# Performance work log

Hardware: AMD Instinct MI355X
Metric: run time of the kernel (lower is better)

The kernel has to match this reference:

```python
import jax, jax.numpy as jnp
import numpy as np

D_IN = 1024
D_OUT = 1024
NUM_HEADS = 16
HEAD_DIM = D_OUT // NUM_HEADS
SCALE = HEAD_DIM ** -0.5


def setup_inputs() -> dict:
    key = jax.random.key(0)
    k_x, k_qkv, k_pw, k_pb = jax.random.split(key, 4)
    B, S = 2, 2048
    x = jax.random.normal(k_x, (B, S, D_IN), dtype=jnp.float32)
    # nn.Linear weights: stored as (out_features, in_features); qkv_bias=False
    w_qkv = jax.random.normal(k_qkv, (3 * D_OUT, D_IN), dtype=jnp.float32) * (D_IN ** -0.5)
    w_proj = jax.random.normal(k_pw, (D_OUT, D_OUT), dtype=jnp.float32) * (D_OUT ** -0.5)
    b_proj = jax.random.normal(k_pb, (D_OUT,), dtype=jnp.float32) * 0.01
    return {"x": x, "w_qkv": w_qkv, "w_proj": w_proj, "b_proj": b_proj}


def reference(x, w_qkv, w_proj, b_proj):
    B, S, _ = x.shape
    # combined QKV projection: (B,S,3*d_out)
    qkv = jnp.einsum('bsd,ed->bse', x, w_qkv)
    qkv = qkv.reshape(B, S, 3, NUM_HEADS, HEAD_DIM)
    qkv = jnp.transpose(qkv, (2, 0, 3, 1, 4))  # (3,B,H,S,hd)
    q, k, v = qkv[0], qkv[1], qkv[2]
    scores = jnp.einsum('bhqd,bhkd->bhqk', q, k)  # (B,H,S,S)
    causal = jnp.triu(jnp.ones((S, S), dtype=bool), k=1)
    # module masks to -inf first, then scales (softmax-equivalent)
    scores = jnp.where(causal, -jnp.inf, scores) * SCALE
    attn = jax.nn.softmax(scores, axis=-1)
    ctx = jnp.einsum('bhqk,bhkd->bhqd', attn, v)
    ctx = jnp.transpose(ctx, (0, 2, 1, 3)).reshape(B, S, D_OUT)
    return jnp.einsum('bsd,ed->bse', ctx, w_proj) + b_proj
```

## Files before the change

### kernel.cpp

```cpp
#include <hip/hip_runtime.h>

#define SEQ    2048
#define NHEAD  16
#define HDIM   64
#define DMODEL 1024
#define BATCH  2

typedef __bf16 bf16;
typedef __bf16 bf16x8 __attribute__((ext_vector_type(8)));
typedef __bf16 bf16x4v __attribute__((ext_vector_type(4)));
typedef float  f32x4  __attribute__((ext_vector_type(4)));

typedef const __attribute__((address_space(1))) void* gas_ptr;
typedef __attribute__((address_space(3))) void*       las_ptr;

__device__ __forceinline__ f32x4 mfma16(bf16x8 a, bf16x8 b, f32x4 c) {
  return __builtin_amdgcn_mfma_f32_16x16x32_bf16(a, b, c, 0, 0, 0);
}

__device__ __forceinline__ void gload_lds16(const void* g, void* l) {
  __builtin_amdgcn_global_load_lds((gas_ptr)(unsigned long long)g,
                                   (las_ptr)(unsigned long long)l, 16, 0, 0);
}

__global__ void convert_all(const float* __restrict__ x, const float* __restrict__ wq,
                            const float* __restrict__ wp, bf16* __restrict__ out) {
  const long long NX = 4194304, NQ = 3145728, NP = 1048576;
  long long i = ((long long)blockIdx.x * blockDim.x + threadIdx.x) * 4;
  if (i >= NX + NQ + NP) return;
  const float* src; long long off;
  if (i < NX)           { src = x;  off = i; }
  else if (i < NX + NQ) { src = wq; off = i - NX; }
  else                  { src = wp; off = i - NX - NQ; }
  float4 f = *reinterpret_cast<const float4*>(src + off);
  bf16x4v r;
  r[0] = (bf16)f.x; r[1] = (bf16)f.y; r[2] = (bf16)f.z; r[3] = (bf16)f.w;
  *reinterpret_cast<bf16x4v*>(out + i) = r;
}

template <int EPI>
__global__ __launch_bounds__(256) void gemm_bt(
    const bf16* __restrict__ A, const bf16* __restrict__ B, int K,
    bf16* __restrict__ q, bf16* __restrict__ k, bf16* __restrict__ v,
    const float* __restrict__ bias, float* __restrict__ out) {
  __shared__ alignas(16) bf16 As[2][128 * 32];
  __shared__ alignas(16) bf16 Bs[2][128 * 32];

  const int tid = threadIdx.x;
  const int l = tid & 63, w = tid >> 6;
  const int lr = l & 15, lg = l >> 4;
  const int wr = (w >> 1) * 64, wc = (w & 1) * 64;
  const long long m0 = (long long)blockIdx.x * 128;
  const long long n0 = (long long)blockIdx.y * 128;
  const int crow = tid >> 2, ccol = (tid & 3) * 8;

  auto stage = [&](int kt, int buf) {
    const bf16* a_src = A + (m0 + crow) * K + (long long)kt * 32 + ccol;
    const bf16* b_src = B + (n0 + crow) * K + (long long)kt * 32 + ccol;
    gload_lds16(a_src,           &As[buf][tid * 8]);
    gload_lds16(a_src + 64LL * K, &As[buf][(tid + 256) * 8]);
    gload_lds16(b_src,           &Bs[buf][tid * 8]);
    gload_lds16(b_src + 64LL * K, &Bs[buf][(tid + 256) * 8]);
  };

  f32x4 acc[4][4];
  const f32x4 fz = {0.f, 0.f, 0.f, 0.f};
#pragma unroll
  for (int m = 0; m < 4; ++m)
#pragma unroll
    for (int n = 0; n < 4; ++n) acc[m][n] = fz;

  stage(0, 0);
  const int nk = K >> 5;
  int cur = 0;
  for (int kt = 0; kt < nk; ++kt) {
    __syncthreads();
    if (kt + 1 < nk) stage(kt + 1, cur ^ 1);
    bf16x8 af[4], bfv[4];
#pragma unroll
    for (int m = 0; m < 4; ++m)
      af[m] = *reinterpret_cast<const bf16x8*>(&As[cur][(wr + m * 16 + lr) * 32 + lg * 8]);
#pragma unroll
    for (int n = 0; n < 4; ++n)
      bfv[n] = *reinterpret_cast<const bf16x8*>(&Bs[cur][(wc + n * 16 + lr) * 32 + lg * 8]);
#pragma unroll
    for (int m = 0; m < 4; ++m)
#pragma unroll
      for (int n = 0; n < 4; ++n) acc[m][n] = mfma16(af[m], bfv[n], acc[m][n]);
    cur ^= 1;
  }

#pragma unroll
  for (int m = 0; m < 4; ++m) {
#pragma unroll
    for (int n = 0; n < 4; ++n) {
#pragma unroll
      for (int j = 0; j < 4; ++j) {
        long long grow = m0 + wr + m * 16 + lg * 4 + j;
        long long gcol = n0 + wc + n * 16 + lr;
        float val = acc[m][n][j];
        if (EPI == 0) {
          int three = (int)(gcol >> 10);
          int rem = (int)(gcol & 1023);
          int h = rem >> 6, d = rem & 63;
          int b = (int)(grow >> 11), s = (int)(grow & 2047);
          int bh = b * NHEAD + h;
          if (three < 2) {
            int dst = ((bh * 128 + (s >> 4)) * 2 + (d >> 5)) * 512 +
                      (s & 15) * 32 + ((d >> 3) & 3) * 8 + (d & 7);
            if (three == 0) q[dst] = (bf16)(val * 0.125f);
            else            k[dst] = (bf16)val;
          } else {
            int dst = (((bh * 4 + (d >> 4)) * 32 + (s >> 6)) * 2 + ((s >> 5) & 1)) * 512 +
                      (d & 15) * 32 + ((s >> 3) & 3) * 8 + (s & 7);
            v[dst] = (bf16)val;
          }
        } else {
          out[grow * 1024 + gcol] = val + bias[gcol];
        }
      }
    }
  }
}

__global__ __launch_bounds__(256, 2) void attn_kernel(
    const bf16* __restrict__ qbuf, const bf16* __restrict__ kbuf,
    const bf16* __restrict__ vbuf, bf16* __restrict__ ctx) {
  const int lid = blockIdx.y * gridDim.x + blockIdx.x;
  const int xcd = lid & 7;
  const int idx = lid >> 3;
  const int bh  = xcd + (idx >> 4) * 8;
  const int p   = idx & 15;
  const int tid = threadIdx.x;
  const int l = tid & 63, w = tid >> 6;
  const int lr = l & 15, lg = l >> 4;
  const int foff = lr * 32 + lg * 8;

  __shared__ alignas(16) bf16 Pl[4][16][72];

  const bf16* Kb = kbuf + bh * 131072 + foff;
  const bf16* Vb = vbuf + bh * 131072 + foff;
  const int b = bh >> 4, h = bh & 15;
  const f32x4 fz = {0.f, 0.f, 0.f, 0.f};

#pragma unroll
  for (int phase = 0; phase < 2; ++phase) {
    const int qg = phase ? (31 - p) : p;
    const int qt16 = qg * 4 + w;
    const int qr0 = qt16 * 16;

    const bf16* Qb = qbuf + (bh * 128 + qt16) * 1024 + foff;
    bf16x8 qf[2];
    qf[0] = *reinterpret_cast<const bf16x8*>(Qb);
    qf[1] = *reinterpret_cast<const bf16x8*>(Qb + 512);

    f32x4 o[4];
    float mrow[4], lrow[4];
#pragma unroll
    for (int nd = 0; nd < 4; ++nd) o[nd] = fz;
#pragma unroll
    for (int j = 0; j < 4; ++j) { mrow[j] = -1e30f; lrow[j] = 0.f; }

    for (int kt = 0; kt <= qg; ++kt) {
      const bool diag = (kt == qg);

      bf16x8 vf[4][2];
#pragma unroll
      for (int nd = 0; nd < 4; ++nd)
#pragma unroll
        for (int kk = 0; kk < 2; ++kk)
          vf[nd][kk] = *reinterpret_cast<const bf16x8*>(
              &Vb[((nd * 32 + kt) * 2 + kk) * 512]);

      bf16x8 kf[4][2];
#pragma unroll
      for (int n = 0; n < 4; ++n)
#pragma unroll
        for (int kk = 0; kk < 2; ++kk)
          kf[n][kk] = *reinterpret_cast<const bf16x8*>(
              &Kb[((kt * 4 + n) * 2 + kk) * 512]);

      f32x4 s4[4];
#pragma unroll
      for (int n = 0; n < 4; ++n)
        s4[n] = mfma16(qf[1], kf[n][1], mfma16(qf[0], kf[n][0], fz));
      if (diag) {
#pragma unroll
        for (int n = 0; n < 4; ++n)
#pragma unroll
          for (int j = 0; j < 4; ++j)
            if (n * 16 + lr > w * 16 + lg * 4 + j) s4[n][j] = -1e30f;
      }

      float pm[4];
#pragma unroll
      for (int j = 0; j < 4; ++j)
        pm[j] = fmaxf(fmaxf(s4[0][j], s4[1][j]), fmaxf(s4[2][j], s4[3][j]));
#pragma unroll
      for (int msk = 1; msk <= 8; msk <<= 1)
#pragma unroll
        for (int j = 0; j < 4; ++j) pm[j] = fmaxf(pm[j], __shfl_xor(pm[j], msk, 64));
      float alpha[4], rs[4];
#pragma unroll
      for (int j = 0; j < 4; ++j) {
        float mn = fmaxf(mrow[j], pm[j]);
        alpha[j] = __expf(mrow[j] - mn);
        mrow[j] = mn;
        rs[j] = 0.f;
      }
#pragma unroll
      for (int n = 0; n < 4; ++n)
#pragma unroll
        for (int j = 0; j < 4; ++j) {
          float pv = __expf(s4[n][j] - mrow[j]);
          s4[n][j] = pv;
          rs[j] += pv;
        }
#pragma unroll
      for (int msk = 1; msk <= 8; msk <<= 1)
#pragma unroll
        for (int j = 0; j < 4; ++j) rs[j] += __shfl_xor(rs[j], msk, 64);
#pragma unroll
      for (int j = 0; j < 4; ++j) lrow[j] = lrow[j] * alpha[j] + rs[j];
#pragma unroll
      for (int nd = 0; nd < 4; ++nd)
#pragma unroll
        for (int j = 0; j < 4; ++j) o[nd][j] *= alpha[j];

#pragma unroll
      for (int n = 0; n < 4; ++n)
#pragma unroll
        for (int j = 0; j < 4; ++j)
          Pl[w][lg * 4 + j][n * 16 + lr] = (bf16)s4[n][j];

#pragma unroll
      for (int kk = 0; kk < 2; ++kk) {
        bf16x8 pf = *reinterpret_cast<const bf16x8*>(&Pl[w][lr][kk * 32 + lg * 8]);
#pragma unroll
        for (int nd = 0; nd < 4; ++nd)
          o[nd] = mfma16(pf, vf[nd][kk], o[nd]);
      }
    }

    float inv[4];
#pragma unroll
    for (int j = 0; j < 4; ++j) inv[j] = 1.0f / lrow[j];
#pragma unroll
    for (int nd = 0; nd < 4; ++nd)
#pragma unroll
      for (int j = 0; j < 4; ++j) {
        int srow = qr0 + lg * 4 + j;
        int d = nd * 16 + lr;
        ctx[((long long)(b * SEQ + srow)) * DMODEL + h * HDIM + d] =
            (bf16)(o[nd][j] * inv[j]);
      }
  }
}

extern "C" void kernel_launch(void* const* d_in, const int* in_sizes, int n_in,
                              void* d_out, int out_size, void* d_ws, size_t ws_size,
                              hipStream_t stream) {
  const float* x      = (const float*)d_in[0];
  const float* w_qkv  = (const float*)d_in[1];
  const float* w_proj = (const float*)d_in[2];
  const float* b_proj = (const float*)d_in[3];
  float* out = (float*)d_out;

  bf16* ws = (bf16*)d_ws;
  bf16* xb     = ws;
  bf16* wqkvb  = xb + 4194304;
  bf16* wprojb = wqkvb + 3145728;
  bf16* qb     = wprojb + 1048576;
  bf16* kb     = qb + 4194304;
  bf16* vb     = kb + 4194304;
  bf16* ctxb   = vb + 4194304;

  convert_all<<<8192, 256, 0, stream>>>(x, w_qkv, w_proj, xb);
  gemm_bt<0><<<dim3(32, 24), 256, 0, stream>>>(xb, wqkvb, 1024, qb, kb, vb, nullptr, nullptr);
  attn_kernel<<<dim3(16, 32), 256, 0, stream>>>(qb, kb, vb, ctxb);
  gemm_bt<1><<<dim3(32, 8), 256, 0, stream>>>(ctxb, wprojb, 1024, nullptr, nullptr, nullptr,
                                              b_proj, out);
}
```

Before: 200.1 us.

## Software-pipeline K/V register loads across a flattened two-phase attention loop

Flattens the two causal query-tile phases into one 33-iteration loop and double-buffers the K and V fragments in registers, loading the next tile's data while the current tile's MFMAs and softmax run. It also defers the cross-lane row-sum reduction to the end of each query tile instead of doing it every iteration. The aim is to hide global load latency and remove per-iteration shuffles, at the cost of twice the register footprint for K/V fragments, which may lower occupancy or cause spills.

```diff
diff --git a/kernel.cpp b/kernel.cpp
--- a/kernel.cpp
+++ b/kernel.cpp
@@ -143,117 +143,135 @@
   const int b = bh >> 4, h = bh & 15;
   const f32x4 fz = {0.f, 0.f, 0.f, 0.f};
 
-#pragma unroll
-  for (int phase = 0; phase < 2; ++phase) {
-    const int qg = phase ? (31 - p) : p;
-    const int qt16 = qg * 4 + w;
-    const int qr0 = qt16 * 16;
-
-    const bf16* Qb = qbuf + (bh * 128 + qt16) * 1024 + foff;
-    bf16x8 qf[2];
-    qf[0] = *reinterpret_cast<const bf16x8*>(Qb);
-    qf[1] = *reinterpret_cast<const bf16x8*>(Qb + 512);
-
-    f32x4 o[4];
-    float mrow[4], lrow[4];
-#pragma unroll
-    for (int nd = 0; nd < 4; ++nd) o[nd] = fz;
-#pragma unroll
-    for (int j = 0; j < 4; ++j) { mrow[j] = -1e30f; lrow[j] = 0.f; }
-
-    for (int kt = 0; kt <= qg; ++kt) {
-      const bool diag = (kt == qg);
-
-      bf16x8 vf[4][2];
+  f32x4 o[4];
+  float mrow[4], lsum[4];
+  bf16x8 qf[2];
+
+  bf16x8 kA[4][2], vA[4][2], kB[4][2], vB[4][2];
+
+#pragma unroll
+  for (int nd = 0; nd < 4; ++nd)
+#pragma unroll
+    for (int kk = 0; kk < 2; ++kk) {
+      vA[nd][kk] = *reinterpret_cast<const bf16x8*>(&Vb[((nd * 32 + 0) * 2 + kk) * 512]);
+      kA[nd][kk] = *reinterpret_cast<const bf16x8*>(&Kb[((0 * 4 + nd) * 2 + kk) * 512]);
+    }
+
+  auto step = [&](bf16x8 (&kc)[4][2], bf16x8 (&vc)[4][2],
+                  bf16x8 (&kn)[4][2], bf16x8 (&vn)[4][2], int i) {
+    const bool in_a = (i <= p);
+    const int qt = in_a ? p : 31 - p;
+    const int kt = in_a ? i : i - p - 1;
+    const bool diag = (kt == qt);
+
+    if (kt == 0) {
+      const int qt16 = qt * 4 + w;
+      const bf16* Qb = qbuf + (bh * 128 + qt16) * 1024 + foff;
+      qf[0] = *reinterpret_cast<const bf16x8*>(Qb);
+      qf[1] = *reinterpret_cast<const bf16x8*>(Qb + 512);
+#pragma unroll
+      for (int nd = 0; nd < 4; ++nd) o[nd] = fz;
+#pragma unroll
+      for (int j = 0; j < 4; ++j) { mrow[j] = -1e30f; lsum[j] = 0.f; }
+    }
+
+    {
+      const int i2 = i + 1;
+      int kt2 = (i2 <= p) ? i2 : i2 - p - 1;
+      if (i2 > 32) kt2 = 0;
 #pragma unroll
       for (int nd = 0; nd < 4; ++nd)
 #pragma unroll
-        for (int kk = 0; kk < 2; ++kk)
-          vf[nd][kk] = *reinterpret_cast<const bf16x8*>(
-              &Vb[((nd * 32 + kt) * 2 + kk) * 512]);
-
-      bf16x8 kf[4][2];
+        for (int kk = 0; kk < 2; ++kk) {
+          vn[nd][kk] = *reinterpret_cast<const bf16x8*>(&Vb[((nd * 32 + kt2) * 2 + kk) * 512]);
+          kn[nd][kk] = *reinterpret_cast<const bf16x8*>(&Kb[((kt2 * 4 + nd) * 2 + kk) * 512]);
+        }
+    }
+
+    f32x4 s4[4];
+#pragma unroll
+    for (int n = 0; n < 4; ++n)
+      s4[n] = mfma16(qf[1], kc[n][1], mfma16(qf[0], kc[n][0], fz));
+    if (diag) {
 #pragma unroll
       for (int n = 0; n < 4; ++n)
 #pragma unroll
-        for (int kk = 0; kk < 2; ++kk)
-          kf[n][kk] = *reinterpret_cast<const bf16x8*>(
-              &Kb[((kt * 4 + n) * 2 + kk) * 512]);
-
-      f32x4 s4[4];
-#pragma unroll
-      for (int n = 0; n < 4; ++n)
-        s4[n] = mfma16(qf[1], kf[n][1], mfma16(qf[0], kf[n][0], fz));
-      if (diag) {
-#pragma unroll
-        for (int n = 0; n < 4; ++n)
-#pragma unroll
-          for (int j = 0; j < 4; ++j)
-            if (n * 16 + lr > w * 16 + lg * 4 + j) s4[n][j] = -1e30f;
+        for (int j = 0; j < 4; ++j)
+          if (n * 16 + lr > w * 16 + lg * 4 + j) s4[n][j] = -1e30f;
+    }
+
+    float pm[4];
+#pragma unroll
+    for (int j = 0; j < 4; ++j)
+      pm[j] = fmaxf(fmaxf(s4[0][j], s4[1][j]), fmaxf(s4[2][j], s4[3][j]));
+#pragma unroll
+    for (int msk = 1; msk <= 8; msk <<= 1)
+#pragma unroll
+      for (int j = 0; j < 4; ++j) pm[j] = fmaxf(pm[j], __shfl_xor(pm[j], msk, 64));
+    float alpha[4];
+#pragma unroll
+    for (int j = 0; j < 4; ++j) {
+      float mn = fmaxf(mrow[j], pm[j]);
+      alpha[j] = __expf(mrow[j] - mn);
+      mrow[j] = mn;
+    }
+    float rs[4] = {0.f, 0.f, 0.f, 0.f};
+#pragma unroll
+    for (int n = 0; n < 4; ++n)
+#pragma unroll
+      for (int j = 0; j < 4; ++j) {
+        float pv = __expf(s4[n][j] - mrow[j]);
+        s4[n][j] = pv;
+        rs[j] += pv;
       }
-
-      float pm[4];
+#pragma unroll
+    for (int j = 0; j < 4; ++j) lsum[j] = lsum[j] * alpha[j] + rs[j];
+#pragma unroll
+    for (int nd = 0; nd < 4; ++nd)
+#pragma unroll
+      for (int j = 0; j < 4; ++j) o[nd][j] *= alpha[j];
+
+#pragma unroll
+    for (int n = 0; n < 4; ++n)
 #pragma unroll
       for (int j = 0; j < 4; ++j)
-        pm[j] = fmaxf(fmaxf(s4[0][j], s4[1][j]), fmaxf(s4[2][j], s4[3][j]));
+        Pl[w][lg * 4 + j][n * 16 + lr] = (bf16)s4[n][j];
+
+#pragma unroll
+    for (int kk = 0; kk < 2; ++kk) {
+      bf16x8 pf = *reinterpret_cast<const bf16x8*>(&Pl[w][lr][kk * 32 + lg * 8]);
+#pragma unroll
+      for (int nd = 0; nd < 4; ++nd)
+        o[nd] = mfma16(pf, vc[nd][kk], o[nd]);
+    }
+
+    if (diag) {
+      float ls[4];
+#pragma unroll
+      for (int j = 0; j < 4; ++j) ls[j] = lsum[j];
 #pragma unroll
       for (int msk = 1; msk <= 8; msk <<= 1)
 #pragma unroll
-        for (int j = 0; j < 4; ++j) pm[j] = fmaxf(pm[j], __shfl_xor(pm[j], msk, 64));
-      float alpha[4], rs[4];
-#pragma unroll
-      for (int j = 0; j < 4; ++j) {
-        float mn = fmaxf(mrow[j], pm[j]);
-        alpha[j] = __expf(mrow[j] - mn);
-        mrow[j] = mn;
-        rs[j] = 0.f;
-      }
-#pragma unroll
-      for (int n = 0; n < 4; ++n)
+        for (int j = 0; j < 4; ++j) ls[j] += __shfl_xor(ls[j], msk, 64);
+      float inv[4];
+#pragma unroll
+      for (int j = 0; j < 4; ++j) inv[j] = 1.0f / ls[j];
+      const int qr0 = (qt * 4 + w) * 16;
+#pragma unroll
+      for (int nd = 0; nd < 4; ++nd)
 #pragma unroll
         for (int j = 0; j < 4; ++j) {
-          float pv = __expf(s4[n][j] - mrow[j]);
-          s4[n][j] = pv;
-          rs[j] += pv;
+          int srow = qr0 + lg * 4 + j;
+          int d = nd * 16 + lr;
+          ctx[((long long)(b * SEQ + srow)) * DMODEL + h * HDIM + d] =
+              (bf16)(o[nd][j] * inv[j]);
         }
-#pragma unroll
-      for (int msk = 1; msk <= 8; msk <<= 1)
-#pragma unroll
-        for (int j = 0; j < 4; ++j) rs[j] += __shfl_xor(rs[j], msk, 64);
-#pragma unroll
-      for (int j = 0; j < 4; ++j) lrow[j] = lrow[j] * alpha[j] + rs[j];
-#pragma unroll
-      for (int nd = 0; nd < 4; ++nd)
-#pragma unroll
-        for (int j = 0; j < 4; ++j) o[nd][j] *= alpha[j];
-
-#pragma unroll
-      for (int n = 0; n < 4; ++n)
-#pragma unroll
-        for (int j = 0; j < 4; ++j)
-          Pl[w][lg * 4 + j][n * 16 + lr] = (bf16)s4[n][j];
-
-#pragma unroll
-      for (int kk = 0; kk < 2; ++kk) {
-        bf16x8 pf = *reinterpret_cast<const bf16x8*>(&Pl[w][lr][kk * 32 + lg * 8]);
-#pragma unroll
-        for (int nd = 0; nd < 4; ++nd)
-          o[nd] = mfma16(pf, vf[nd][kk], o[nd]);
-      }
-    }
-
-    float inv[4];
-#pragma unroll
-    for (int j = 0; j < 4; ++j) inv[j] = 1.0f / lrow[j];
-#pragma unroll
-    for (int nd = 0; nd < 4; ++nd)
-#pragma unroll
-      for (int j = 0; j < 4; ++j) {
-        int srow = qr0 + lg * 4 + j;
-        int d = nd * 16 + lr;
-        ctx[((long long)(b * SEQ + srow)) * DMODEL + h * HDIM + d] =
-            (bf16)(o[nd][j] * inv[j]);
-      }
+    }
+  };
+
+  for (int i = 0; i < 33; i += 2) {
+    step(kA, vA, kB, vB, i);
+    if (i + 1 < 33) step(kB, vB, kA, vA, i + 1);
   }
 }
 
```

Result: no change. 200.5 us (+0.2%).

## Split attention KV range across two wave halves and merge partial softmax

Applied to the files above, without the earlier changes.

Doubles the attention block to 512 threads. Each query tile's key range is split between two groups of four waves, and the partial outputs, maxima and sums are merged through shared memory at the end (split-K style flash attention). The per-iteration cross-lane row-sum reduction moves out of the loop to a single reduction at the end. This adds parallelism and cuts per-wave serial work, at the cost of extra LDS, two barriers per phase and a tighter register budget from the 512,4 launch bounds.

```diff
diff --git a/kernel.cpp b/kernel.cpp
--- a/kernel.cpp
+++ b/kernel.cpp
@@ -123,7 +123,7 @@
   }
 }
 
-__global__ __launch_bounds__(256, 2) void attn_kernel(
+__global__ __launch_bounds__(512, 4) void attn_kernel(
     const bf16* __restrict__ qbuf, const bf16* __restrict__ kbuf,
     const bf16* __restrict__ vbuf, bf16* __restrict__ ctx) {
   const int lid = blockIdx.y * gridDim.x + blockIdx.x;
@@ -133,10 +133,14 @@
   const int p   = idx & 15;
   const int tid = threadIdx.x;
   const int l = tid & 63, w = tid >> 6;
+  const int wt = w & 3;
+  const int half = w >> 2;
   const int lr = l & 15, lg = l >> 4;
   const int foff = lr * 32 + lg * 8;
 
-  __shared__ alignas(16) bf16 Pl[4][16][72];
+  __shared__ alignas(16) bf16  Pl[8][16][72];
+  __shared__ alignas(16) float Om[4][16][68];
+  __shared__ float Mm[4][16], Lm[4][16];
 
   const bf16* Kb = kbuf + bh * 131072 + foff;
   const bf16* Vb = vbuf + bh * 131072 + foff;
@@ -146,8 +150,11 @@
 #pragma unroll
   for (int phase = 0; phase < 2; ++phase) {
     const int qg = phase ? (31 - p) : p;
-    const int qt16 = qg * 4 + w;
-    const int qr0 = qt16 * 16;
+    const int nk = qg + 1;
+    const int hs = (nk + 1) >> 1;
+    const int klo = half ? hs : 0;
+    const int khi = half ? nk : hs;
+    const int qt16 = qg * 4 + wt;
 
     const bf16* Qb = qbuf + (bh * 128 + qt16) * 1024 + foff;
     bf16x8 qf[2];
@@ -155,13 +162,13 @@
     qf[1] = *reinterpret_cast<const bf16x8*>(Qb + 512);
 
     f32x4 o[4];
-    float mrow[4], lrow[4];
+    float mrow[4], lsum[4];
 #pragma unroll
     for (int nd = 0; nd < 4; ++nd) o[nd] = fz;
 #pragma unroll
-    for (int j = 0; j < 4; ++j) { mrow[j] = -1e30f; lrow[j] = 0.f; }
-
-    for (int kt = 0; kt <= qg; ++kt) {
+    for (int j = 0; j < 4; ++j) { mrow[j] = -1e30f; lsum[j] = 0.f; }
+
+    for (int kt = klo; kt < khi; ++kt) {
       const bool diag = (kt == qg);
 
       bf16x8 vf[4][2];
@@ -189,7 +196,7 @@
         for (int n = 0; n < 4; ++n)
 #pragma unroll
           for (int j = 0; j < 4; ++j)
-            if (n * 16 + lr > w * 16 + lg * 4 + j) s4[n][j] = -1e30f;
+            if (n * 16 + lr > wt * 16 + lg * 4 + j) s4[n][j] = -1e30f;
       }
 
       float pm[4];
@@ -200,14 +207,14 @@
       for (int msk = 1; msk <= 8; msk <<= 1)
 #pragma unroll
         for (int j = 0; j < 4; ++j) pm[j] = fmaxf(pm[j], __shfl_xor(pm[j], msk, 64));
-      float alpha[4], rs[4];
+      float alpha[4];
 #pragma unroll
       for (int j = 0; j < 4; ++j) {
         float mn = fmaxf(mrow[j], pm[j]);
         alpha[j] = __expf(mrow[j] - mn);
         mrow[j] = mn;
-        rs[j] = 0.f;
-      }
+      }
+      float rs[4] = {0.f, 0.f, 0.f, 0.f};
 #pragma unroll
       for (int n = 0; n < 4; ++n)
 #pragma unroll
@@ -217,11 +224,7 @@
           rs[j] += pv;
         }
 #pragma unroll
-      for (int msk = 1; msk <= 8; msk <<= 1)
-#pragma unroll
-        for (int j = 0; j < 4; ++j) rs[j] += __shfl_xor(rs[j], msk, 64);
-#pragma unroll
-      for (int j = 0; j < 4; ++j) lrow[j] = lrow[j] * alpha[j] + rs[j];
+      for (int j = 0; j < 4; ++j) lsum[j] = lsum[j] * alpha[j] + rs[j];
 #pragma unroll
       for (int nd = 0; nd < 4; ++nd)
 #pragma unroll
@@ -242,18 +245,53 @@
       }
     }
 
-    float inv[4];
-#pragma unroll
-    for (int j = 0; j < 4; ++j) inv[j] = 1.0f / lrow[j];
-#pragma unroll
-    for (int nd = 0; nd < 4; ++nd)
+    float ls[4];
+#pragma unroll
+    for (int j = 0; j < 4; ++j) ls[j] = lsum[j];
+#pragma unroll
+    for (int msk = 1; msk <= 8; msk <<= 1)
+#pragma unroll
+      for (int j = 0; j < 4; ++j) ls[j] += __shfl_xor(ls[j], msk, 64);
+
+    if (half) {
+#pragma unroll
+      for (int nd = 0; nd < 4; ++nd)
+#pragma unroll
+        for (int j = 0; j < 4; ++j)
+          Om[wt][lg * 4 + j][nd * 16 + lr] = o[nd][j];
+      if (lr == 0) {
+#pragma unroll
+        for (int j = 0; j < 4; ++j) {
+          Mm[wt][lg * 4 + j] = mrow[j];
+          Lm[wt][lg * 4 + j] = ls[j];
+        }
+      }
+    }
+    __syncthreads();
+    if (!half) {
+      float wA[4], wB[4], inv[4];
 #pragma unroll
       for (int j = 0; j < 4; ++j) {
-        int srow = qr0 + lg * 4 + j;
-        int d = nd * 16 + lr;
-        ctx[((long long)(b * SEQ + srow)) * DMODEL + h * HDIM + d] =
-            (bf16)(o[nd][j] * inv[j]);
-      }
+        float mB = Mm[wt][lg * 4 + j];
+        float lB = Lm[wt][lg * 4 + j];
+        float mM = fmaxf(mrow[j], mB);
+        wA[j] = __expf(mrow[j] - mM);
+        wB[j] = __expf(mB - mM);
+        inv[j] = 1.0f / (ls[j] * wA[j] + lB * wB[j]);
+      }
+      const int qr0 = qt16 * 16;
+#pragma unroll
+      for (int nd = 0; nd < 4; ++nd)
+#pragma unroll
+        for (int j = 0; j < 4; ++j) {
+          float oB = Om[wt][lg * 4 + j][nd * 16 + lr];
+          int srow = qr0 + lg * 4 + j;
+          int d = nd * 16 + lr;
+          ctx[((long long)(b * SEQ + srow)) * DMODEL + h * HDIM + d] =
+              (bf16)((o[nd][j] * wA[j] + oB * wB[j]) * inv[j]);
+        }
+    }
+    __syncthreads();
   }
 }
 
@@ -277,7 +315,7 @@
 
   convert_all<<<8192, 256, 0, stream>>>(x, w_qkv, w_proj, xb);
   gemm_bt<0><<<dim3(32, 24), 256, 0, stream>>>(xb, wqkvb, 1024, qb, kb, vb, nullptr, nullptr);
-  attn_kernel<<<dim3(16, 32), 256, 0, stream>>>(qb, kb, vb, ctxb);
+  attn_kernel<<<dim3(16, 32), 512, 0, stream>>>(qb, kb, vb, ctxb);
   gemm_bt<1><<<dim3(32, 8), 256, 0, stream>>>(ctxb, wprojb, 1024, nullptr, nullptr, nullptr,
                                               b_proj, out);
 }
```

New measurement: 203.0 us. Within noise of the previous version (+1.5%).
